# Optimization experiments

Measured on AMD Instinct MI355X. Metric: run time of the kernel, lower is better.

## Reference

```python
import jax, jax.numpy as jnp
import numpy as np
from jax import lax

# Norse default LIF/LI parameters with dt=0.001
DT_TAU_MEM = 0.1   # dt * tau_mem_inv (1/1e-2)
DT_TAU_SYN = 0.2   # dt * tau_syn_inv (1/5e-3)
V_TH = 0.5
ALPHA = 100.0      # SuperSpike surrogate slope (backward only)

@jax.custom_vjp
def spike(x):
    return (x > 0).astype(x.dtype)

def _spike_fwd(x):
    return (x > 0).astype(x.dtype), x

def _spike_bwd(x, g):
    # SuperSpike surrogate gradient: 1 / (alpha*|x| + 1)^2
    sg = 1.0 / (ALPHA * jnp.abs(x) + 1.0) ** 2
    return (g * sg,)

spike.defvjp(_spike_fwd, _spike_bwd)

def setup_inputs() -> dict:
    key = jax.random.key(0)
    k1, k2, k3 = jax.random.split(key, 3)
    T, B, C, H, W = 64, 512, 1, 28, 28
    IN, HID, OUT = 784, 2048, 10
    x = jax.random.normal(k1, (T, B, C, H, W), dtype=jnp.float32)
    # Kaiming-uniform-ish bias-free Linear weights, torch layout [out, in]
    w1 = jax.random.uniform(k2, (HID, IN), jnp.float32, -1.0, 1.0) / np.sqrt(IN)
    w_out = jax.random.uniform(k3, (OUT, HID), jnp.float32, -1.0, 1.0) / np.sqrt(HID)
    return {"x": x, "w1": w1, "w_out": w_out}

def reference(x, w1, w_out):
    T, B = x.shape[0], x.shape[1]
    HID, OUT = w1.shape[0], w_out.shape[0]
    xf = x.reshape(T, B, -1)  # [T, B, IN]

    def step(carry, xt):
        v1, i1, vo, io = carry
        cur = xt @ w1.T                       # fc1: [B, HID]
        # LIF: decay, threshold/spike/reset, then integrate new input current
        v1_dec = v1 + DT_TAU_MEM * (-v1 + i1)
        i1_dec = i1 * (1.0 - DT_TAU_SYN)
        z = spike(v1_dec - V_TH)
        v1_new = (1.0 - z) * v1_dec           # v_reset = 0
        i1_new = i1_dec + cur
        out_cur = z @ w_out.T                 # fc_out: [B, OUT]
        # LI readout: leaky integration (no spiking)
        vo_new = vo + DT_TAU_MEM * (-vo + io)
        io_new = io * (1.0 - DT_TAU_SYN) + out_cur
        return (v1_new, i1_new, vo_new, io_new), vo_new

    zh = jnp.zeros((B, HID), x.dtype)
    zo = jnp.zeros((B, OUT), x.dtype)
    _, voltages = lax.scan(step, (zh, zh, zo, zo), xf)  # [T, B, OUT]
    return jnp.max(voltages, axis=0)
```

## Files before the change

kernel.cpp:

```cpp
#include <hip/hip_runtime.h>
#include <cstdint>
#include <cstddef>

#define T_STEPS 64
#define BATCH 512
#define IN_F 784
#define KP 800
#define HID 2048
#define OUT_F 10

#define DEC_V 0.9f
#define DEC_I 0.8f
#define DT_V 0.1f
#define V_TH 0.5f

typedef __attribute__((ext_vector_type(8))) _Float16 f16x8;
typedef __attribute__((ext_vector_type(4))) _Float16 f16x4;
typedef __attribute__((ext_vector_type(4))) float f32x4;

__device__ __forceinline__ void load_lds16(const _Float16* g, _Float16* l) {
  __builtin_amdgcn_global_load_lds(
      (const __attribute__((address_space(1))) void*)g,
      (__attribute__((address_space(3))) void*)l, 16, 0, 0);
}

__global__ __launch_bounds__(256)
void split_rows(const float* __restrict__ src, _Float16* __restrict__ hi,
                _Float16* __restrict__ lo) {
  const int row = blockIdx.x * 2 + (threadIdx.x >> 7);
  const int ln = threadIdx.x & 127;
  const float4* s = (const float4*)(src + (size_t)row * IN_F);
#pragma unroll
  for (int it = 0; it < 2; ++it) {
    const int q = ln + it * 128;
    if (q >= 200) break;
    float4 v = (q < 196) ? s[q] : make_float4(0.f, 0.f, 0.f, 0.f);
    f16x4 h, l;
    h.x = (_Float16)v.x; l.x = (_Float16)(v.x - (float)h.x);
    h.y = (_Float16)v.y; l.y = (_Float16)(v.y - (float)h.y);
    h.z = (_Float16)v.z; l.z = (_Float16)(v.z - (float)h.z);
    h.w = (_Float16)v.w; l.w = (_Float16)(v.w - (float)h.w);
    *(f16x4*)&hi[(size_t)row * KP + q * 4] = h;
    *(f16x4*)&lo[(size_t)row * KP + q * 4] = l;
  }
}

__global__ __launch_bounds__(256, 4)
void gemm_fc1(const _Float16* __restrict__ Ah, const _Float16* __restrict__ Al,
              const _Float16* __restrict__ Wh, const _Float16* __restrict__ Wl,
              float* __restrict__ C) {
  __shared__ _Float16 sAh[128 * 32];
  __shared__ _Float16 sAl[128 * 32];
  __shared__ _Float16 sWh[128 * 32];
  __shared__ _Float16 sWl[128 * 32];

  const int tid = threadIdx.x;
  const int lane = tid & 63;
  const int wv = tid >> 6;
  const int bn = blockIdx.x * 128;
  const int bm = blockIdx.y * 128;

  const int sr = lane >> 2;
  const int skc = (lane & 3) * 8;

  const int wr = (wv >> 1) * 64;
  const int wc = (wv & 1) * 64;
  const int col = lane & 15;
  const int quad = lane >> 4;

  f32x4 acc[4][4] = {};

  const size_t arow = (size_t)(bm + wv * 32 + sr) * KP + skc;
  const size_t wrow = (size_t)(bn + wv * 32 + sr) * KP + skc;

  for (int k0 = 0; k0 < KP; k0 += 32) {
    __syncthreads();
#pragma unroll
    for (int j = 0; j < 2; ++j) {
      const int ro = wv * 32 + j * 16;
      load_lds16(Ah + arow + (size_t)j * 16 * KP + k0, sAh + ro * 32);
      load_lds16(Al + arow + (size_t)j * 16 * KP + k0, sAl + ro * 32);
      load_lds16(Wh + wrow + (size_t)j * 16 * KP + k0, sWh + ro * 32);
      load_lds16(Wl + wrow + (size_t)j * 16 * KP + k0, sWl + ro * 32);
    }
    __syncthreads();

    f16x8 fah[4], fal[4], fwh[4], fwl[4];
#pragma unroll
    for (int i = 0; i < 4; ++i) {
      fah[i] = *(const f16x8*)&sAh[(wr + i * 16 + col) * 32 + quad * 8];
      fal[i] = *(const f16x8*)&sAl[(wr + i * 16 + col) * 32 + quad * 8];
      fwh[i] = *(const f16x8*)&sWh[(wc + i * 16 + col) * 32 + quad * 8];
      fwl[i] = *(const f16x8*)&sWl[(wc + i * 16 + col) * 32 + quad * 8];
    }
#pragma unroll
    for (int mi = 0; mi < 4; ++mi)
#pragma unroll
      for (int ni = 0; ni < 4; ++ni) {
        acc[mi][ni] = __builtin_amdgcn_mfma_f32_16x16x32_f16(fah[mi], fwh[ni], acc[mi][ni], 0, 0, 0);
        acc[mi][ni] = __builtin_amdgcn_mfma_f32_16x16x32_f16(fah[mi], fwl[ni], acc[mi][ni], 0, 0, 0);
        acc[mi][ni] = __builtin_amdgcn_mfma_f32_16x16x32_f16(fal[mi], fwh[ni], acc[mi][ni], 0, 0, 0);
      }
  }

#pragma unroll
  for (int mi = 0; mi < 4; ++mi)
#pragma unroll
    for (int ni = 0; ni < 4; ++ni)
#pragma unroll
      for (int r = 0; r < 4; ++r) {
        const int row = bm + wr + mi * 16 + quad * 4 + r;
        const int cg = bn + wc + ni * 16 + col;
        C[(size_t)row * HID + cg] = acc[mi][ni][r];
      }
}

__global__ __launch_bounds__(256)
void lif_out(const float* __restrict__ cur, const float* __restrict__ wo,
             float* __restrict__ v1, float* __restrict__ i1,
             float* __restrict__ outP, int tc, int t0) {
  __shared__ _Float16 zL[T_STEPS][264];
  __shared__ _Float16 wT[16][264];

  const int tid = threadIdx.x;
  const int hc = blockIdx.x;
  const int b = blockIdx.y;
  const int hb = hc * 256;

  for (int i = tid; i < 16 * 256; i += 256) {
    const int n = i >> 8, k = i & 255;
    wT[n][k] = (n < OUT_F) ? (_Float16)wo[(size_t)n * HID + hb + k] : (_Float16)0.f;
  }

  const int sidx = b * HID + hb + tid;
  float v = v1[sidx];
  float ci = i1[sidx];
#pragma unroll 4
  for (int t = 0; t < tc; ++t) {
    const float c = cur[(size_t)t * (BATCH * HID) + sidx];
    const float vd = DEC_V * v + DT_V * ci;
    const float z = (vd > V_TH) ? 1.0f : 0.0f;
    v = (1.0f - z) * vd;
    ci = DEC_I * ci + c;
    zL[t][tid] = (_Float16)z;
  }
  v1[sidx] = v;
  i1[sidx] = ci;
  __syncthreads();

  const int wv = tid >> 6;
  const int lane = tid & 63;
  const int col = lane & 15;
  const int quad = lane >> 4;
  f32x4 acc = {};
  const _Float16* za = &zL[wv * 16 + col][0];
  const _Float16* wb = &wT[col][0];
#pragma unroll
  for (int ks = 0; ks < 8; ++ks) {
    f16x8 a = *(const f16x8*)(za + ks * 32 + quad * 8);
    f16x8 bb = *(const f16x8*)(wb + ks * 32 + quad * 8);
    acc = __builtin_amdgcn_mfma_f32_16x16x32_f16(a, bb, acc, 0, 0, 0);
  }
  if (col < OUT_F) {
#pragma unroll
    for (int r = 0; r < 4; ++r) {
      const int t = wv * 16 + quad * 4 + r;
      if (t < tc)
        outP[(((size_t)hc * T_STEPS + (t0 + t)) * BATCH + b) * OUT_F + col] = acc[r];
    }
  }
}

__global__ __launch_bounds__(256)
void li_scan(const float* __restrict__ outP, float* __restrict__ out) {
  const int idx = blockIdx.x * 256 + threadIdx.x;
  if (idx >= BATCH * OUT_F) return;
  float vo = 0.f, io = 0.f, vmax = 0.f;
  for (int t = 0; t < T_STEPS; ++t) {
    float oc = 0.f;
#pragma unroll
    for (int hc = 0; hc < 8; ++hc)
      oc += outP[((size_t)hc * T_STEPS + t) * (BATCH * OUT_F) + idx];
    const float von = DEC_V * vo + DT_V * io;
    io = DEC_I * io + oc;
    vo = von;
    vmax = fmaxf(vmax, von);
  }
  out[idx] = vmax;
}

__global__ void zero_state(float* __restrict__ p, int n) {
  int i = blockIdx.x * 256 + threadIdx.x;
  if (i < n) p[i] = 0.0f;
}

extern "C" void kernel_launch(void* const* d_in, const int* in_sizes, int n_in,
                              void* d_out, int out_size, void* d_ws, size_t ws_size,
                              hipStream_t stream) {
  const float* x  = (const float*)d_in[0];
  const float* w1 = (const float*)d_in[1];
  const float* wo = (const float*)d_in[2];
  float* out = (float*)d_out;

  const size_t BH = (size_t)BATCH * HID;

  float* v1 = (float*)d_ws;
  float* i1 = v1 + BH;
  float* outP = i1 + BH;
  _Float16* WhG = (_Float16*)(outP + (size_t)8 * T_STEPS * BATCH * OUT_F);
  _Float16* WlG = WhG + (size_t)HID * KP;
  char* chunk0 = (char*)(WlG + (size_t)HID * KP);

  const size_t base_bytes = (size_t)(chunk0 - (char*)d_ws);
  const size_t per_step = BH * 4 + (size_t)2 * BATCH * KP * 2;
  int Tc = 1;
  if (ws_size > base_bytes + per_step) {
    size_t m = (ws_size - base_bytes) / per_step;
    Tc = (m >= T_STEPS) ? T_STEPS : (int)m;
  }

  float* cur = (float*)chunk0;
  _Float16* AhC = (_Float16*)(cur + (size_t)Tc * BH);
  _Float16* AlC = AhC + (size_t)Tc * BATCH * KP;

  split_rows<<<HID / 2, 256, 0, stream>>>(w1, WhG, WlG);
  zero_state<<<(int)((2 * BH + 255) / 256), 256, 0, stream>>>(v1, (int)(2 * BH));

  for (int t0 = 0; t0 < T_STEPS; t0 += Tc) {
    const int tc = (T_STEPS - t0 < Tc) ? (T_STEPS - t0) : Tc;
    const int nrows = tc * BATCH;
    split_rows<<<nrows / 2, 256, 0, stream>>>(x + (size_t)t0 * BATCH * IN_F, AhC, AlC);
    dim3 grid(HID / 128, nrows / 128);
    gemm_fc1<<<grid, 256, 0, stream>>>(AhC, AlC, WhG, WlG, cur);
    dim3 lgrid(HID / 256, BATCH);
    lif_out<<<lgrid, 256, 0, stream>>>(cur, wo, v1, i1, outP, tc, t0);
  }
  li_scan<<<(BATCH * OUT_F + 255) / 256, 256, 0, stream>>>(outP, out);
}
```

Measured before the change: 639.5 us.

## Fuse fp32-to-fp16 hi/lo split of activations into the fc1 GEMM

```diff
diff --git a/kernel.cpp b/kernel.cpp
--- a/kernel.cpp
+++ b/kernel.cpp
@@ -16,17 +16,23 @@
 
 typedef __attribute__((ext_vector_type(8))) _Float16 f16x8;
 typedef __attribute__((ext_vector_type(4))) _Float16 f16x4;
+typedef __attribute__((ext_vector_type(2))) __fp16 fp16v2;
 typedef __attribute__((ext_vector_type(4))) float f32x4;
 
-__device__ __forceinline__ void load_lds16(const _Float16* g, _Float16* l) {
+__device__ __forceinline__ void load_lds16h(const _Float16* g, _Float16* l) {
   __builtin_amdgcn_global_load_lds(
       (const __attribute__((address_space(1))) void*)g,
       (__attribute__((address_space(3))) void*)l, 16, 0, 0);
 }
+__device__ __forceinline__ void load_lds16f(const float* g, float* l) {
+  __builtin_amdgcn_global_load_lds(
+      (const __attribute__((address_space(1))) void*)g,
+      (__attribute__((address_space(3))) void*)l, 16, 0, 0);
+}
 
 __global__ __launch_bounds__(256)
-void split_rows(const float* __restrict__ src, _Float16* __restrict__ hi,
-                _Float16* __restrict__ lo) {
+void split_w(const float* __restrict__ src, _Float16* __restrict__ hi,
+             _Float16* __restrict__ lo) {
   const int row = blockIdx.x * 2 + (threadIdx.x >> 7);
   const int ln = threadIdx.x & 127;
   const float4* s = (const float4*)(src + (size_t)row * IN_F);
@@ -45,14 +51,12 @@
   }
 }
 
-__global__ __launch_bounds__(256, 4)
-void gemm_fc1(const _Float16* __restrict__ Ah, const _Float16* __restrict__ Al,
-              const _Float16* __restrict__ Wh, const _Float16* __restrict__ Wl,
-              float* __restrict__ C) {
-  __shared__ _Float16 sAh[128 * 32];
-  __shared__ _Float16 sAl[128 * 32];
-  __shared__ _Float16 sWh[128 * 32];
-  __shared__ _Float16 sWl[128 * 32];
+__global__ __launch_bounds__(256, 2)
+void gemm_fc1(const float* __restrict__ A, const _Float16* __restrict__ Wh,
+              const _Float16* __restrict__ Wl, float* __restrict__ C) {
+  __shared__ float    sA [8 * 512];
+  __shared__ _Float16 sWh[8 * 512];
+  __shared__ _Float16 sWl[8 * 512];
 
   const int tid = threadIdx.x;
   const int lane = tid & 63;
@@ -60,38 +64,79 @@
   const int bn = blockIdx.x * 128;
   const int bm = blockIdx.y * 128;
 
-  const int sr = lane >> 2;
-  const int skc = (lane & 3) * 8;
+  const int srow = lane & 15;
+  const int sq = lane >> 4;
+
+  const int t0i = wv * 2, t1i = wv * 2 + 1;
+  const float*    a0 = A  + (size_t)(bm + t0i * 16 + srow) * IN_F + sq * 8;
+  const float*    a1 = A  + (size_t)(bm + t1i * 16 + srow) * IN_F + sq * 8;
+  const _Float16* h0 = Wh + (size_t)(bn + t0i * 16 + srow) * KP + sq * 8;
+  const _Float16* h1 = Wh + (size_t)(bn + t1i * 16 + srow) * KP + sq * 8;
+  const _Float16* l0 = Wl + (size_t)(bn + t0i * 16 + srow) * KP + sq * 8;
+  const _Float16* l1 = Wl + (size_t)(bn + t1i * 16 + srow) * KP + sq * 8;
 
   const int wr = (wv >> 1) * 64;
   const int wc = (wv & 1) * 64;
   const int col = lane & 15;
   const int quad = lane >> 4;
+  const int wrT = wr >> 4, wcT = wc >> 4;
 
   f32x4 acc[4][4] = {};
-
-  const size_t arow = (size_t)(bm + wv * 32 + sr) * KP + skc;
-  const size_t wrow = (size_t)(bn + wv * 32 + sr) * KP + skc;
 
   for (int k0 = 0; k0 < KP; k0 += 32) {
     __syncthreads();
-#pragma unroll
-    for (int j = 0; j < 2; ++j) {
-      const int ro = wv * 32 + j * 16;
-      load_lds16(Ah + arow + (size_t)j * 16 * KP + k0, sAh + ro * 32);
-      load_lds16(Al + arow + (size_t)j * 16 * KP + k0, sAl + ro * 32);
-      load_lds16(Wh + wrow + (size_t)j * 16 * KP + k0, sWh + ro * 32);
-      load_lds16(Wl + wrow + (size_t)j * 16 * KP + k0, sWl + ro * 32);
+    const bool tail = (k0 + 32 > IN_F);
+    if (!tail) {
+      load_lds16f(a0 + k0,     sA + t0i * 512);
+      load_lds16f(a0 + k0 + 4, sA + t0i * 512 + 256);
+      load_lds16f(a1 + k0,     sA + t1i * 512);
+      load_lds16f(a1 + k0 + 4, sA + t1i * 512 + 256);
+    } else {
+      if (sq >= 2) {
+        const float4 z4 = make_float4(0.f, 0.f, 0.f, 0.f);
+        *(float4*)&sA[t0i * 512 +       lane * 4] = z4;
+        *(float4*)&sA[t0i * 512 + 256 + lane * 4] = z4;
+        *(float4*)&sA[t1i * 512 +       lane * 4] = z4;
+        *(float4*)&sA[t1i * 512 + 256 + lane * 4] = z4;
+      } else {
+        load_lds16f(a0 + k0,     sA + t0i * 512);
+        load_lds16f(a0 + k0 + 4, sA + t0i * 512 + 256);
+        load_lds16f(a1 + k0,     sA + t1i * 512);
+        load_lds16f(a1 + k0 + 4, sA + t1i * 512 + 256);
+      }
     }
+    load_lds16h(h0 + k0, sWh + t0i * 512);
+    load_lds16h(l0 + k0, sWl + t0i * 512);
+    load_lds16h(h1 + k0, sWh + t1i * 512);
+    load_lds16h(l1 + k0, sWl + t1i * 512);
     __syncthreads();
 
     f16x8 fah[4], fal[4], fwh[4], fwl[4];
 #pragma unroll
     for (int i = 0; i < 4; ++i) {
-      fah[i] = *(const f16x8*)&sAh[(wr + i * 16 + col) * 32 + quad * 8];
-      fal[i] = *(const f16x8*)&sAl[(wr + i * 16 + col) * 32 + quad * 8];
-      fwh[i] = *(const f16x8*)&sWh[(wc + i * 16 + col) * 32 + quad * 8];
-      fwl[i] = *(const f16x8*)&sWl[(wc + i * 16 + col) * 32 + quad * 8];
+      fwh[i] = *(const f16x8*)&sWh[(wcT + i) * 512 + lane * 8];
+      fwl[i] = *(const f16x8*)&sWl[(wcT + i) * 512 + lane * 8];
+      const float4 p0 = *(const float4*)&sA[(wrT + i) * 512 +       lane * 4];
+      const float4 p1 = *(const float4*)&sA[(wrT + i) * 512 + 256 + lane * 4];
+      const float hx0 = __uint_as_float(__float_as_uint(p0.x) & 0xffffe000u);
+      const float hy0 = __uint_as_float(__float_as_uint(p0.y) & 0xffffe000u);
+      const float hz0 = __uint_as_float(__float_as_uint(p0.z) & 0xffffe000u);
+      const float hw0 = __uint_as_float(__float_as_uint(p0.w) & 0xffffe000u);
+      const float hx1 = __uint_as_float(__float_as_uint(p1.x) & 0xffffe000u);
+      const float hy1 = __uint_as_float(__float_as_uint(p1.y) & 0xffffe000u);
+      const float hz1 = __uint_as_float(__float_as_uint(p1.z) & 0xffffe000u);
+      const float hw1 = __uint_as_float(__float_as_uint(p1.w) & 0xffffe000u);
+      union { f16x8 v; fp16v2 h[4]; } uh, ul;
+      uh.h[0] = __builtin_amdgcn_cvt_pkrtz(hx0, hy0);
+      uh.h[1] = __builtin_amdgcn_cvt_pkrtz(hz0, hw0);
+      uh.h[2] = __builtin_amdgcn_cvt_pkrtz(hx1, hy1);
+      uh.h[3] = __builtin_amdgcn_cvt_pkrtz(hz1, hw1);
+      ul.h[0] = __builtin_amdgcn_cvt_pkrtz(p0.x - hx0, p0.y - hy0);
+      ul.h[1] = __builtin_amdgcn_cvt_pkrtz(p0.z - hz0, p0.w - hw0);
+      ul.h[2] = __builtin_amdgcn_cvt_pkrtz(p1.x - hx1, p1.y - hy1);
+      ul.h[3] = __builtin_amdgcn_cvt_pkrtz(p1.z - hz1, p1.w - hw1);
+      fah[i] = uh.v;
+      fal[i] = ul.v;
     }
 #pragma unroll
     for (int mi = 0; mi < 4; ++mi)
@@ -209,29 +254,21 @@
   float* outP = i1 + BH;
   _Float16* WhG = (_Float16*)(outP + (size_t)8 * T_STEPS * BATCH * OUT_F);
   _Float16* WlG = WhG + (size_t)HID * KP;
-  char* chunk0 = (char*)(WlG + (size_t)HID * KP);
-
-  const size_t base_bytes = (size_t)(chunk0 - (char*)d_ws);
-  const size_t per_step = BH * 4 + (size_t)2 * BATCH * KP * 2;
-  int Tc = 1;
-  if (ws_size > base_bytes + per_step) {
-    size_t m = (ws_size - base_bytes) / per_step;
-    Tc = (m >= T_STEPS) ? T_STEPS : (int)m;
-  }
-
-  float* cur = (float*)chunk0;
-  _Float16* AhC = (_Float16*)(cur + (size_t)Tc * BH);
-  _Float16* AlC = AhC + (size_t)Tc * BATCH * KP;
-
-  split_rows<<<HID / 2, 256, 0, stream>>>(w1, WhG, WlG);
+  float* cur = (float*)(WlG + (size_t)HID * KP);
+
+  const size_t base_bytes = (size_t)((char*)cur - (char*)d_ws);
+  const size_t per_step = BH * sizeof(float);
+  int Tc = T_STEPS;
+  while (Tc > 1 && base_bytes + (size_t)Tc * per_step > ws_size) Tc >>= 1;
+
+  split_w<<<HID / 2, 256, 0, stream>>>(w1, WhG, WlG);
   zero_state<<<(int)((2 * BH + 255) / 256), 256, 0, stream>>>(v1, (int)(2 * BH));
 
   for (int t0 = 0; t0 < T_STEPS; t0 += Tc) {
     const int tc = (T_STEPS - t0 < Tc) ? (T_STEPS - t0) : Tc;
     const int nrows = tc * BATCH;
-    split_rows<<<nrows / 2, 256, 0, stream>>>(x + (size_t)t0 * BATCH * IN_F, AhC, AlC);
     dim3 grid(HID / 128, nrows / 128);
-    gemm_fc1<<<grid, 256, 0, stream>>>(AhC, AlC, WhG, WlG, cur);
+    gemm_fc1<<<grid, 256, 0, stream>>>(x + (size_t)t0 * BATCH * IN_F, WhG, WlG, cur);
     dim3 lgrid(HID / 256, BATCH);
     lif_out<<<lgrid, 256, 0, stream>>>(cur, wo, v1, i1, outP, tc, t0);
   }
```

After: 657.1 us. 2.8% more time.

## Pre-swizzle split-fp16 operands into MFMA fragment layout and widen GEMM tile

Applied to the files above, without the earlier changes.

```diff
diff --git a/kernel.cpp b/kernel.cpp
--- a/kernel.cpp
+++ b/kernel.cpp
@@ -5,7 +5,7 @@
 #define T_STEPS 64
 #define BATCH 512
 #define IN_F 784
-#define KP 800
+#define NKT 25
 #define HID 2048
 #define OUT_F 10
 
@@ -15,104 +15,115 @@
 #define V_TH 0.5f
 
 typedef __attribute__((ext_vector_type(8))) _Float16 f16x8;
-typedef __attribute__((ext_vector_type(4))) _Float16 f16x4;
 typedef __attribute__((ext_vector_type(4))) float f32x4;
 
-__device__ __forceinline__ void load_lds16(const _Float16* g, _Float16* l) {
+__device__ __forceinline__ void load_lds16h(const _Float16* g, _Float16* l) {
   __builtin_amdgcn_global_load_lds(
       (const __attribute__((address_space(1))) void*)g,
       (__attribute__((address_space(3))) void*)l, 16, 0, 0);
 }
 
 __global__ __launch_bounds__(256)
-void split_rows(const float* __restrict__ src, _Float16* __restrict__ hi,
-                _Float16* __restrict__ lo) {
-  const int row = blockIdx.x * 2 + (threadIdx.x >> 7);
-  const int ln = threadIdx.x & 127;
-  const float4* s = (const float4*)(src + (size_t)row * IN_F);
-#pragma unroll
-  for (int it = 0; it < 2; ++it) {
-    const int q = ln + it * 128;
-    if (q >= 200) break;
-    float4 v = (q < 196) ? s[q] : make_float4(0.f, 0.f, 0.f, 0.f);
-    f16x4 h, l;
-    h.x = (_Float16)v.x; l.x = (_Float16)(v.x - (float)h.x);
-    h.y = (_Float16)v.y; l.y = (_Float16)(v.y - (float)h.y);
-    h.z = (_Float16)v.z; l.z = (_Float16)(v.z - (float)h.z);
-    h.w = (_Float16)v.w; l.w = (_Float16)(v.w - (float)h.w);
-    *(f16x4*)&hi[(size_t)row * KP + q * 4] = h;
-    *(f16x4*)&lo[(size_t)row * KP + q * 4] = l;
-  }
-}
-
-__global__ __launch_bounds__(256, 4)
-void gemm_fc1(const _Float16* __restrict__ Ah, const _Float16* __restrict__ Al,
-              const _Float16* __restrict__ Wh, const _Float16* __restrict__ Wl,
+void split_frag(const float* __restrict__ src, _Float16* __restrict__ hiT,
+                _Float16* __restrict__ loT) {
+  __shared__ float xr[16][804];
+  const int mt = blockIdx.x;
+  for (int i = threadIdx.x; i < 16 * IN_F; i += 256) {
+    const int r = i / IN_F, c = i - r * IN_F;
+    xr[r][c] = src[(size_t)(mt * 16 + r) * IN_F + c];
+  }
+  for (int i = threadIdx.x; i < 16 * 16; i += 256)
+    xr[i >> 4][IN_F + (i & 15)] = 0.0f;
+  __syncthreads();
+
+  const int l = threadIdx.x & 63;
+  const int g = threadIdx.x >> 6;
+  const int r = l & 15, q = l >> 4;
+  for (int kt = g; kt < NKT; kt += 4) {
+    const float* s = &xr[r][kt * 32 + q * 8];
+    f16x8 h, lo;
+#pragma unroll
+    for (int j = 0; j < 8; ++j) {
+      const float v = s[j];
+      const _Float16 hh = (_Float16)v;
+      h[j] = hh;
+      lo[j] = (_Float16)(v - (float)hh);
+    }
+    const size_t off = ((size_t)mt * NKT + kt) * 512 + l * 8;
+    *(f16x8*)&hiT[off] = h;
+    *(f16x8*)&loT[off] = lo;
+  }
+}
+
+__global__ __launch_bounds__(256, 2)
+void gemm_fc1(const _Float16* __restrict__ AhT, const _Float16* __restrict__ AlT,
+              const _Float16* __restrict__ WhT, const _Float16* __restrict__ WlT,
               float* __restrict__ C) {
-  __shared__ _Float16 sAh[128 * 32];
-  __shared__ _Float16 sAl[128 * 32];
-  __shared__ _Float16 sWh[128 * 32];
-  __shared__ _Float16 sWl[128 * 32];
+  __shared__ _Float16 __attribute__((aligned(16))) sAh[8 * 512];
+  __shared__ _Float16 __attribute__((aligned(16))) sAl[8 * 512];
+  __shared__ _Float16 __attribute__((aligned(16))) sWh[16 * 512];
+  __shared__ _Float16 __attribute__((aligned(16))) sWl[16 * 512];
 
   const int tid = threadIdx.x;
   const int lane = tid & 63;
   const int wv = tid >> 6;
-  const int bn = blockIdx.x * 128;
-  const int bm = blockIdx.y * 128;
-
-  const int sr = lane >> 2;
-  const int skc = (lane & 3) * 8;
-
-  const int wr = (wv >> 1) * 64;
-  const int wc = (wv & 1) * 64;
+  const int bmT = blockIdx.y * 8;
+  const int bnT = blockIdx.x * 16;
+
+  const int wrT = (wv >> 1) * 4;
+  const int wcT = (wv & 1) * 8;
   const int col = lane & 15;
   const int quad = lane >> 4;
 
-  f32x4 acc[4][4] = {};
-
-  const size_t arow = (size_t)(bm + wv * 32 + sr) * KP + skc;
-  const size_t wrow = (size_t)(bn + wv * 32 + sr) * KP + skc;
-
-  for (int k0 = 0; k0 < KP; k0 += 32) {
+  f32x4 acc[4][8] = {};
+
+  for (int kt = 0; kt < NKT; ++kt) {
     __syncthreads();
 #pragma unroll
     for (int j = 0; j < 2; ++j) {
-      const int ro = wv * 32 + j * 16;
-      load_lds16(Ah + arow + (size_t)j * 16 * KP + k0, sAh + ro * 32);
-      load_lds16(Al + arow + (size_t)j * 16 * KP + k0, sAl + ro * 32);
-      load_lds16(Wh + wrow + (size_t)j * 16 * KP + k0, sWh + ro * 32);
-      load_lds16(Wl + wrow + (size_t)j * 16 * KP + k0, sWl + ro * 32);
+      const int t = wv * 2 + j;
+      const size_t go = ((size_t)(bmT + t) * NKT + kt) * 512 + lane * 8;
+      load_lds16h(AhT + go, sAh + t * 512);
+      load_lds16h(AlT + go, sAl + t * 512);
+    }
+#pragma unroll
+    for (int j = 0; j < 4; ++j) {
+      const int t = wv * 4 + j;
+      const size_t go = ((size_t)(bnT + t) * NKT + kt) * 512 + lane * 8;
+      load_lds16h(WhT + go, sWh + t * 512);
+      load_lds16h(WlT + go, sWl + t * 512);
     }
     __syncthreads();
 
-    f16x8 fah[4], fal[4], fwh[4], fwl[4];
+    f16x8 fah[4], fal[4];
 #pragma unroll
     for (int i = 0; i < 4; ++i) {
-      fah[i] = *(const f16x8*)&sAh[(wr + i * 16 + col) * 32 + quad * 8];
-      fal[i] = *(const f16x8*)&sAl[(wr + i * 16 + col) * 32 + quad * 8];
-      fwh[i] = *(const f16x8*)&sWh[(wc + i * 16 + col) * 32 + quad * 8];
-      fwl[i] = *(const f16x8*)&sWl[(wc + i * 16 + col) * 32 + quad * 8];
-    }
-#pragma unroll
-    for (int mi = 0; mi < 4; ++mi)
-#pragma unroll
-      for (int ni = 0; ni < 4; ++ni) {
-        acc[mi][ni] = __builtin_amdgcn_mfma_f32_16x16x32_f16(fah[mi], fwh[ni], acc[mi][ni], 0, 0, 0);
-        acc[mi][ni] = __builtin_amdgcn_mfma_f32_16x16x32_f16(fah[mi], fwl[ni], acc[mi][ni], 0, 0, 0);
-        acc[mi][ni] = __builtin_amdgcn_mfma_f32_16x16x32_f16(fal[mi], fwh[ni], acc[mi][ni], 0, 0, 0);
+      fah[i] = *(const f16x8*)&sAh[(wrT + i) * 512 + lane * 8];
+      fal[i] = *(const f16x8*)&sAl[(wrT + i) * 512 + lane * 8];
+    }
+#pragma unroll
+    for (int ni = 0; ni < 8; ++ni) {
+      const f16x8 fwh = *(const f16x8*)&sWh[(wcT + ni) * 512 + lane * 8];
+      const f16x8 fwl = *(const f16x8*)&sWl[(wcT + ni) * 512 + lane * 8];
+#pragma unroll
+      for (int mi = 0; mi < 4; ++mi) {
+        acc[mi][ni] = __builtin_amdgcn_mfma_f32_16x16x32_f16(fah[mi], fwh, acc[mi][ni], 0, 0, 0);
+        acc[mi][ni] = __builtin_amdgcn_mfma_f32_16x16x32_f16(fah[mi], fwl, acc[mi][ni], 0, 0, 0);
+        acc[mi][ni] = __builtin_amdgcn_mfma_f32_16x16x32_f16(fal[mi], fwh, acc[mi][ni], 0, 0, 0);
       }
-  }
-
+    }
+  }
+
+  const int rowb = blockIdx.y * 128 + (wv >> 1) * 64;
+  const int colb = blockIdx.x * 256 + (wv & 1) * 128;
 #pragma unroll
   for (int mi = 0; mi < 4; ++mi)
 #pragma unroll
-    for (int ni = 0; ni < 4; ++ni)
-#pragma unroll
-      for (int r = 0; r < 4; ++r) {
-        const int row = bm + wr + mi * 16 + quad * 4 + r;
-        const int cg = bn + wc + ni * 16 + col;
-        C[(size_t)row * HID + cg] = acc[mi][ni][r];
-      }
+    for (int ni = 0; ni < 8; ++ni)
+#pragma unroll
+      for (int r = 0; r < 4; ++r)
+        C[(size_t)(rowb + mi * 16 + quad * 4 + r) * HID + colb + ni * 16 + col] =
+            acc[mi][ni][r];
 }
 
 __global__ __launch_bounds__(256)
@@ -203,35 +214,33 @@
   float* out = (float*)d_out;
 
   const size_t BH = (size_t)BATCH * HID;
+  const size_t WT_HALVES = (size_t)(HID / 16) * NKT * 512;
 
   float* v1 = (float*)d_ws;
   float* i1 = v1 + BH;
   float* outP = i1 + BH;
-  _Float16* WhG = (_Float16*)(outP + (size_t)8 * T_STEPS * BATCH * OUT_F);
-  _Float16* WlG = WhG + (size_t)HID * KP;
-  char* chunk0 = (char*)(WlG + (size_t)HID * KP);
+  _Float16* WhT = (_Float16*)(outP + (size_t)8 * T_STEPS * BATCH * OUT_F);
+  _Float16* WlT = WhT + WT_HALVES;
+  char* chunk0 = (char*)(WlT + WT_HALVES);
 
   const size_t base_bytes = (size_t)(chunk0 - (char*)d_ws);
-  const size_t per_step = BH * 4 + (size_t)2 * BATCH * KP * 2;
-  int Tc = 1;
-  if (ws_size > base_bytes + per_step) {
-    size_t m = (ws_size - base_bytes) / per_step;
-    Tc = (m >= T_STEPS) ? T_STEPS : (int)m;
-  }
+  const size_t per_step = BH * 4 + (size_t)2 * 32 * NKT * 512 * 2;
+  int Tc = T_STEPS;
+  while (Tc > 1 && base_bytes + (size_t)Tc * per_step > ws_size) Tc >>= 1;
 
   float* cur = (float*)chunk0;
-  _Float16* AhC = (_Float16*)(cur + (size_t)Tc * BH);
-  _Float16* AlC = AhC + (size_t)Tc * BATCH * KP;
-
-  split_rows<<<HID / 2, 256, 0, stream>>>(w1, WhG, WlG);
+  _Float16* AhT = (_Float16*)(cur + (size_t)Tc * BH);
+  _Float16* AlT = AhT + (size_t)Tc * 32 * NKT * 512;
+
+  split_frag<<<HID / 16, 256, 0, stream>>>(w1, WhT, WlT);
   zero_state<<<(int)((2 * BH + 255) / 256), 256, 0, stream>>>(v1, (int)(2 * BH));
 
   for (int t0 = 0; t0 < T_STEPS; t0 += Tc) {
     const int tc = (T_STEPS - t0 < Tc) ? (T_STEPS - t0) : Tc;
     const int nrows = tc * BATCH;
-    split_rows<<<nrows / 2, 256, 0, stream>>>(x + (size_t)t0 * BATCH * IN_F, AhC, AlC);
-    dim3 grid(HID / 128, nrows / 128);
-    gemm_fc1<<<grid, 256, 0, stream>>>(AhC, AlC, WhG, WlG, cur);
+    split_frag<<<nrows / 16, 256, 0, stream>>>(x + (size_t)t0 * BATCH * IN_F, AhT, AlT);
+    dim3 grid(HID / 256, nrows / 128);
+    gemm_fc1<<<grid, 256, 0, stream>>>(AhT, AlT, WhT, WlT, cur);
     dim3 lgrid(HID / 256, BATCH);
     lif_out<<<lgrid, 256, 0, stream>>>(cur, wo, v1, i1, outP, tc, t0);
   }
```

After: 596.4 us. -6.7%, faster.
